# Performance work log

Hardware: AMD Instinct MI355X
Metric: run time of the kernel (lower is better)

The kernel has to match this reference:

```python
import jax, jax.numpy as jnp
import numpy as np

B, S, D_IN, D_HEAD = 4, 4096, 1024, 64

def setup_inputs() -> dict:
    key = jax.random.key(0)
    k1, k2, k3, k4 = jax.random.split(key, 4)
    scale = 0.02
    return {
        "input_vectors": jax.random.normal(k1, (B, S, D_IN), dtype=jnp.float32),
        "Wq": jax.random.normal(k2, (D_IN, D_HEAD), dtype=jnp.float32) * scale,
        "Wk": jax.random.normal(k3, (D_IN, D_HEAD), dtype=jnp.float32) * scale,
        "Wv": jax.random.normal(k4, (D_IN, D_HEAD), dtype=jnp.float32) * scale,
    }

def reference(input_vectors, Wq, Wk, Wv):
    # QKV projections (Linear with no bias): [B,S,d_in] @ [d_in,d_head]
    q = input_vectors @ Wq  # [B,S,H]
    k = input_vectors @ Wk
    v = input_vectors @ Wv
    n = input_vectors.shape[1]
    # causal attention scores: [B,S,S]
    scores = jnp.einsum('bqh,bkh->bqk', q, k)
    causal = jnp.tril(jnp.ones((n, n), dtype=bool))  # True = keep
    scores = jnp.where(causal, scores, -jnp.inf)
    scale = k.shape[-1] ** -0.5
    attn = jax.nn.softmax(scores * scale, axis=-1)
    return jnp.einsum('bqk,bkh->bqh', attn, v)
```

## Files before the change

kernel.cpp:

```cpp
#include <hip/hip_runtime.h>
#include <stdint.h>

#define SEQ   4096
#define DIN   1024

typedef __attribute__((ext_vector_type(8))) short bf16x8;
typedef __attribute__((ext_vector_type(4))) float floatx4;
typedef __attribute__((ext_vector_type(4))) unsigned short ushortx4;

#if __has_builtin(__builtin_amdgcn_exp2f)
#define EXP2(x) __builtin_amdgcn_exp2f(x)
#else
#define EXP2(x) exp2f(x)
#endif

__device__ __forceinline__ unsigned short f2bf(float f) {
    union { float f; unsigned int u; } v; v.f = f;
    unsigned int u = v.u + 0x7fffu + ((v.u >> 16) & 1u);
    return (unsigned short)(u >> 16);
}
__device__ __forceinline__ float bf2f(unsigned short h) {
    union { unsigned int u; float f; } v; v.u = ((unsigned int)h) << 16;
    return v.f;
}
__device__ __forceinline__ float uasf(unsigned int u) {
    union { unsigned int u; float f; } v; v.u = u; return v.f;
}
__device__ __forceinline__ unsigned int fasu(float f) {
    union { float f; unsigned int u; } v; v.f = f; return v.u;
}
__device__ __forceinline__ float dpp_xor1(float x) {
    return uasf((unsigned)__builtin_amdgcn_mov_dpp((int)fasu(x), 0xB1, 0xF, 0xF, true));
}
__device__ __forceinline__ float dpp_xor2(float x) {
    return uasf((unsigned)__builtin_amdgcn_mov_dpp((int)fasu(x), 0x4E, 0xF, 0xF, true));
}

__global__ void wt_prep(const float* __restrict__ Wq, const float* __restrict__ Wk,
                        const float* __restrict__ Wv, unsigned short* __restrict__ WT) {
    int idx = blockIdx.x * 256 + threadIdx.x;
    int n   = idx & 63;
    int k   = (idx >> 6) & 1023;
    int mat = idx >> 16;
    const float* W = (mat == 0) ? Wq : ((mat == 1) ? Wk : Wv);
    WT[(size_t)(mat * 64 + n) * 1024 + k] = f2bf(W[k * 64 + n]);
}

#define QSCALE 0.18033688011112042f
__launch_bounds__(512, 2)
__global__ void proj_qkv(const float* __restrict__ X, const unsigned short* __restrict__ WT,
                         unsigned short* __restrict__ qb, unsigned short* __restrict__ kb,
                         unsigned short* __restrict__ vb) {
    __shared__ __align__(16) float          X0[64 * 64], X1[64 * 64];
    __shared__ __align__(16) unsigned short W0[192 * 64], W1[192 * 64];
    const int tid = threadIdx.x;
    const int wave = tid >> 6, lane = tid & 63;
    const int quad = lane >> 4, l16 = lane & 15;
    const int strip = wave >> 1;
    const int cg = wave & 1;
    const int row0 = blockIdx.x * 64;
    const int m = strip * 16 + l16;

    floatx4 acc[6];
#pragma unroll
    for (int i = 0; i < 6; i++) acc[i] = (floatx4){0.f, 0.f, 0.f, 0.f};

    int xu[2], xr[2], xc[2], wu[3], wr[3], wc[3];
#pragma unroll
    for (int i = 0; i < 2; i++) {
        xu[i] = i * 512 + tid; xr[i] = xu[i] >> 4; xc[i] = (xu[i] & 15) ^ (xr[i] & 15);
    }
#pragma unroll
    for (int i = 0; i < 3; i++) {
        wu[i] = i * 512 + tid; wr[i] = wu[i] >> 3; wc[i] = (wu[i] & 7) ^ (wr[i] & 7);
    }
    floatx4 xpre[2], wpre[3];
    auto issue = [&](int k0) {
#pragma unroll
        for (int i = 0; i < 2; i++)
            xpre[i] = *(const floatx4*)(X + (size_t)(row0 + xr[i]) * DIN + k0 + xc[i] * 4);
#pragma unroll
        for (int i = 0; i < 3; i++)
            wpre[i] = *(const floatx4*)(WT + (size_t)wr[i] * 1024 + k0 + wc[i] * 8);
    };

    issue(0);
    for (int kc = 0; kc < 16; kc++) {
        float*          Xd = (kc & 1) ? X1 : X0;
        unsigned short* Wd = (kc & 1) ? W1 : W0;
#pragma unroll
        for (int i = 0; i < 2; i++) *(floatx4*)&Xd[xu[i] * 4] = xpre[i];
#pragma unroll
        for (int i = 0; i < 3; i++) *(floatx4*)&Wd[wu[i] * 8] = wpre[i];
        if (kc < 15) issue((kc + 1) * 64);
        __syncthreads();

        bf16x8 af[2];
#pragma unroll
        for (int ks = 0; ks < 2; ks++) {
            floatx4 x0 = *(const floatx4*)&Xd[m * 64 + ((ks * 8 + quad * 2 + 0) ^ (m & 15)) * 4];
            floatx4 x1 = *(const floatx4*)&Xd[m * 64 + ((ks * 8 + quad * 2 + 1) ^ (m & 15)) * 4];
#pragma unroll
            for (int j = 0; j < 4; j++) {
                af[ks][j]     = (short)f2bf(x0[j]);
                af[ks][j + 4] = (short)f2bf(x1[j]);
            }
        }
#pragma unroll
        for (int i = 0; i < 6; i++) {
            const int nrow = (cg * 6 + i) * 16 + l16;
#pragma unroll
            for (int ks = 0; ks < 2; ks++) {
                const int c = ks * 4 + quad;
                bf16x8 bfrag = *(const bf16x8*)&Wd[nrow * 64 + (c ^ (nrow & 7)) * 8];
                acc[i] = __builtin_amdgcn_mfma_f32_16x16x32_bf16(af[ks], bfrag, acc[i], 0, 0, 0);
            }
        }
    }
#pragma unroll
    for (int i = 0; i < 6; i++) {
        const int nt = cg * 6 + i;
        const int mat = nt >> 2;
        const int col = (nt & 3) * 16 + l16;
#pragma unroll
        for (int r = 0; r < 4; r++) {
            const int orow = row0 + strip * 16 + quad * 4 + r;
            float v = acc[i][r];
            if (mat == 0) {
                qb[(size_t)orow * 64 + col] = f2bf(v * QSCALE);
            } else if (mat == 1) {
                kb[(size_t)orow * 64 + col] = f2bf(v);
            } else {
                int b = orow >> 12, sq = orow & 4095;
                vb[((size_t)b * 64 + col) * SEQ + sq] = f2bf(v);
            }
        }
    }
}

__launch_bounds__(256, 2)
__global__ void attn(const unsigned short* __restrict__ qb, const unsigned short* __restrict__ kb,
                     const unsigned short* __restrict__ vb, unsigned short* __restrict__ opart,
                     float* __restrict__ lpart) {
    __shared__ __align__(16) unsigned short K0[64 * 64], K1[64 * 64];
    __shared__ __align__(16) unsigned short V0[64 * 64], V1[64 * 64];
    __shared__ __align__(16) unsigned short Pl[4][32 * 72];

    const int bid = blockIdx.x;
    const int batch = bid & 3;
    const int mm = bid >> 2;
    const int rank = (bid < 256) ? (127 - mm) : (mm - 64);
    const int qt = rank >> 2, s = rank & 3;
    const int q0 = qt * 128;
    const int T = 2 * qt + 2;
    const int ktlo = (T * s) >> 2, kthi = (T * (s + 1)) >> 2;

    const int tid = threadIdx.x;
    const int wave = tid >> 6, lane = tid & 63;
    const int quad = lane >> 4, l16 = lane & 15;

    bf16x8 qa[2][2];
#pragma unroll
    for (int rt = 0; rt < 2; rt++) {
        const unsigned short* qr = qb + (size_t)(batch * SEQ + q0 + wave * 32 + rt * 16 + l16) * 64;
        qa[rt][0] = *(const bf16x8*)(qr + quad * 8);
        qa[rt][1] = *(const bf16x8*)(qr + 32 + quad * 8);
    }
    floatx4 o[2][4];
#pragma unroll
    for (int rt = 0; rt < 2; rt++)
#pragma unroll
        for (int nt = 0; nt < 4; nt++) o[rt][nt] = (floatx4){0.f, 0.f, 0.f, 0.f};
    float lsum[2] = {0.f, 0.f};

    const unsigned short* kbase = kb + (size_t)batch * SEQ * 64;
    const unsigned short* vbase = vb + (size_t)batch * 64 * SEQ;

    int ku[2], kr[2], kc_[2], vu[2], vd[2], vc[2];
#pragma unroll
    for (int i = 0; i < 2; i++) {
        ku[i] = i * 256 + tid; kr[i] = ku[i] >> 3; kc_[i] = (ku[i] & 7) ^ (kr[i] & 7);
        vu[i] = i * 256 + tid; vd[i] = vu[i] >> 3; vc[i] = (vu[i] & 7) ^ (vd[i] & 7);
    }
    floatx4 kpre[2], vpre[2];
    auto issue = [&](int k0) {
#pragma unroll
        for (int i = 0; i < 2; i++)
            kpre[i] = *(const floatx4*)(kbase + (size_t)(k0 + kr[i]) * 64 + kc_[i] * 8);
#pragma unroll
        for (int i = 0; i < 2; i++)
            vpre[i] = *(const floatx4*)(vbase + (size_t)vd[i] * SEQ + k0 + vc[i] * 8);
    };

    if (ktlo < kthi) issue(ktlo * 64);
    for (int kt = ktlo; kt < kthi; kt++) {
        unsigned short* Kd = (kt & 1) ? K1 : K0;
        unsigned short* Vd = (kt & 1) ? V1 : V0;
#pragma unroll
        for (int i = 0; i < 2; i++) *(floatx4*)&Kd[ku[i] * 8] = kpre[i];
#pragma unroll
        for (int i = 0; i < 2; i++) *(floatx4*)&Vd[vu[i] * 8] = vpre[i];
        if (kt + 1 < kthi) issue((kt + 1) * 64);
        __syncthreads();

        const int k0 = kt * 64;
        const bool domask = (k0 + 63) > (q0 + wave * 32);
        unsigned short* P = &Pl[wave][0];
#pragma unroll
        for (int rt = 0; rt < 2; rt++) {
            floatx4 sc[4];
#pragma unroll
            for (int nt = 0; nt < 4; nt++) {
                sc[nt] = (floatx4){0.f, 0.f, 0.f, 0.f};
                const int key = nt * 16 + l16;
#pragma unroll
                for (int ks = 0; ks < 2; ks++) {
                    const int c = ks * 4 + quad;
                    bf16x8 bk = *(const bf16x8*)&Kd[key * 64 + (c ^ (key & 7)) * 8];
                    sc[nt] = __builtin_amdgcn_mfma_f32_16x16x32_bf16(qa[rt][ks], bk, sc[nt], 0, 0, 0);
                }
            }
            if (domask) {
#pragma unroll
                for (int nt = 0; nt < 4; nt++) {
                    const int col = k0 + nt * 16 + l16;
#pragma unroll
                    for (int r = 0; r < 4; r++) {
                        const int rowg = q0 + wave * 32 + rt * 16 + quad * 4 + r;
                        if (col > rowg) sc[nt][r] = -1e30f;
                    }
                }
            }
#pragma unroll
            for (int nt = 0; nt < 4; nt++) {
                float v0 = EXP2(sc[nt][0]), v1 = EXP2(sc[nt][1]);
                float v2 = EXP2(sc[nt][2]), v3 = EXP2(sc[nt][3]);
                float t0 = dpp_xor2(v0), t1 = dpp_xor2(v1), t2 = dpp_xor2(v2), t3 = dpp_xor2(v3);
                if (lane & 2) { v0 = t2; v1 = t3; } else { v2 = t0; v3 = t1; }
                t0 = dpp_xor1(v0); t1 = dpp_xor1(v1); t2 = dpp_xor1(v2); t3 = dpp_xor1(v3);
                if (lane & 1) { v0 = t1; v2 = t3; } else { v1 = t0; v3 = t2; }
                unsigned int u0 = fasu(v0) & 0xffff0000u, u1 = fasu(v1) & 0xffff0000u;
                unsigned int u2 = fasu(v2) & 0xffff0000u, u3 = fasu(v3) & 0xffff0000u;
                lsum[rt] += (uasf(u0) + uasf(u1)) + (uasf(u2) + uasf(u3));
                uint2 w;
                w.x = (u0 >> 16) | u1;
                w.y = (u2 >> 16) | u3;
                const int prow = rt * 16 + quad * 4 + (lane & 3);
                const int pcol = nt * 16 + (l16 >> 2) * 4;
                *(uint2*)&P[prow * 72 + pcol] = w;
            }
        }
#pragma unroll
        for (int ks = 0; ks < 2; ks++) {
            bf16x8 pa[2];
#pragma unroll
            for (int rt = 0; rt < 2; rt++)
                pa[rt] = *(const bf16x8*)&P[(rt * 16 + l16) * 72 + ks * 32 + quad * 8];
#pragma unroll
            for (int nt = 0; nt < 4; nt++) {
                const int d = nt * 16 + l16;
                bf16x8 bv = *(const bf16x8*)&Vd[d * 64 + (((ks * 4 + quad)) ^ (d & 7)) * 8];
#pragma unroll
                for (int rt = 0; rt < 2; rt++)
                    o[rt][nt] = __builtin_amdgcn_mfma_f32_16x16x32_bf16(pa[rt], bv, o[rt][nt], 0, 0, 0);
            }
        }
    }

    unsigned short* ob = opart + (size_t)s * (4 * SEQ * 64)
                       + (size_t)(batch * SEQ + q0 + wave * 32) * 64;
    float* lb = lpart + (size_t)s * (4 * SEQ) + (size_t)(batch * SEQ + q0 + wave * 32);
#pragma unroll
    for (int rt = 0; rt < 2; rt++) {
        float l = lsum[rt];
        l += __shfl_xor(l, 4);
        l += __shfl_xor(l, 8);
#pragma unroll
        for (int nt = 0; nt < 4; nt++)
#pragma unroll
            for (int r = 0; r < 4; r++)
                ob[(rt * 16 + quad * 4 + r) * 64 + nt * 16 + l16] = f2bf(o[rt][nt][r]);
        if ((l16 >> 2) == 0) lb[rt * 16 + quad * 4 + (l16 & 3)] = l;
    }
}

__global__ void merge(const unsigned short* __restrict__ opart, const float* __restrict__ lpart,
                      float* __restrict__ out) {
    int idx = blockIdx.x * 256 + threadIdx.x;
    int row = idx >> 4, c4 = idx & 15;
    float l = lpart[row] + lpart[4 * SEQ + row] + lpart[8 * SEQ + row] + lpart[12 * SEQ + row];
    float inv = 1.f / l;
    floatx4 acc = (floatx4){0.f, 0.f, 0.f, 0.f};
#pragma unroll
    for (int s = 0; s < 4; s++) {
        ushortx4 u = *(const ushortx4*)(opart + (size_t)s * (4 * SEQ * 64)
                                        + (size_t)row * 64 + c4 * 4);
#pragma unroll
        for (int j = 0; j < 4; j++) acc[j] += bf2f(u[j]);
    }
    acc *= inv;
    *(floatx4*)(out + (size_t)row * 64 + c4 * 4) = acc;
}

extern "C" void kernel_launch(void* const* d_in, const int* in_sizes, int n_in,
                              void* d_out, int out_size, void* d_ws, size_t ws_size,
                              hipStream_t stream) {
    const float* X  = (const float*)d_in[0];
    const float* Wq = (const float*)d_in[1];
    const float* Wk = (const float*)d_in[2];
    const float* Wv = (const float*)d_in[3];
    float* out = (float*)d_out;
    char* ws = (char*)d_ws;
    unsigned short* WT = (unsigned short*)ws;
    unsigned short* qb = (unsigned short*)(ws + 393216);
    unsigned short* kb = (unsigned short*)(ws + 393216 + 2097152);
    unsigned short* vb = (unsigned short*)(ws + 393216 + 2 * 2097152);
    unsigned short* opart = (unsigned short*)(ws + 393216 + 3 * 2097152);
    float* lpart = (float*)(ws + 393216 + 3 * 2097152 + 8388608);

    hipLaunchKernelGGL(wt_prep,  dim3(768), dim3(256), 0, stream, Wq, Wk, Wv, WT);
    hipLaunchKernelGGL(proj_qkv, dim3(256), dim3(512), 0, stream, X, WT, qb, kb, vb);
    hipLaunchKernelGGL(attn,     dim3(512), dim3(256), 0, stream, qb, kb, vb, opart, lpart);
    hipLaunchKernelGGL(merge,    dim3(1024), dim3(256), 0, stream, opart, lpart, out);
}
```

Before: 139.9 us.

## Fuse all stages into one persistent kernel with grid barriers and dynamic work queue

Result: slower. 261.3 us (+86.8%).

```diff
diff --git a/kernel.cpp b/kernel.cpp
--- a/kernel.cpp
+++ b/kernel.cpp
@@ -3,6 +3,8 @@
 
 #define SEQ   4096
 #define DIN   1024
+#define NBLK  256
+#define NITEMS 1024
 
 typedef __attribute__((ext_vector_type(8))) short bf16x8;
 typedef __attribute__((ext_vector_type(4))) float floatx4;
@@ -36,270 +38,268 @@
     return uasf((unsigned)__builtin_amdgcn_mov_dpp((int)fasu(x), 0x4E, 0xF, 0xF, true));
 }
 
-__global__ void wt_prep(const float* __restrict__ Wq, const float* __restrict__ Wk,
-                        const float* __restrict__ Wv, unsigned short* __restrict__ WT) {
-    int idx = blockIdx.x * 256 + threadIdx.x;
-    int n   = idx & 63;
-    int k   = (idx >> 6) & 1023;
-    int mat = idx >> 16;
-    const float* W = (mat == 0) ? Wq : ((mat == 1) ? Wk : Wv);
-    WT[(size_t)(mat * 64 + n) * 1024 + k] = f2bf(W[k * 64 + n]);
+__device__ __forceinline__ void gbar(unsigned int* c, int tid) {
+    __syncthreads();
+    if (tid == 0) {
+        __threadfence();
+        __hip_atomic_fetch_add(c, 1u, __ATOMIC_RELEASE, __HIP_MEMORY_SCOPE_AGENT);
+        while (__hip_atomic_load(c, __ATOMIC_ACQUIRE, __HIP_MEMORY_SCOPE_AGENT) < NBLK)
+            __builtin_amdgcn_s_sleep(1);
+    }
+    __syncthreads();
 }
 
 #define QSCALE 0.18033688011112042f
-__launch_bounds__(512, 2)
-__global__ void proj_qkv(const float* __restrict__ X, const unsigned short* __restrict__ WT,
-                         unsigned short* __restrict__ qb, unsigned short* __restrict__ kb,
-                         unsigned short* __restrict__ vb) {
-    __shared__ __align__(16) float          X0[64 * 64], X1[64 * 64];
-    __shared__ __align__(16) unsigned short W0[192 * 64], W1[192 * 64];
-    const int tid = threadIdx.x;
+
+__launch_bounds__(512, 4)
+__global__ void mega(const float* __restrict__ X, const float* __restrict__ Wq,
+                     const float* __restrict__ Wk, const float* __restrict__ Wv,
+                     unsigned short* __restrict__ WT, unsigned short* __restrict__ qb,
+                     unsigned short* __restrict__ kb, unsigned short* __restrict__ vb,
+                     unsigned short* __restrict__ opart, float* __restrict__ lpart,
+                     unsigned int* cnt, float* __restrict__ out) {
+    __shared__ __align__(16) char smem[81920];
+    const int tid = threadIdx.x, bid = blockIdx.x;
     const int wave = tid >> 6, lane = tid & 63;
     const int quad = lane >> 4, l16 = lane & 15;
-    const int strip = wave >> 1;
-    const int cg = wave & 1;
-    const int row0 = blockIdx.x * 64;
-    const int m = strip * 16 + l16;
-
-    floatx4 acc[6];
-#pragma unroll
-    for (int i = 0; i < 6; i++) acc[i] = (floatx4){0.f, 0.f, 0.f, 0.f};
-
-    int xu[2], xr[2], xc[2], wu[3], wr[3], wc[3];
-#pragma unroll
-    for (int i = 0; i < 2; i++) {
-        xu[i] = i * 512 + tid; xr[i] = xu[i] >> 4; xc[i] = (xu[i] & 15) ^ (xr[i] & 15);
-    }
-#pragma unroll
-    for (int i = 0; i < 3; i++) {
-        wu[i] = i * 512 + tid; wr[i] = wu[i] >> 3; wc[i] = (wu[i] & 7) ^ (wr[i] & 7);
-    }
-    floatx4 xpre[2], wpre[3];
-    auto issue = [&](int k0) {
-#pragma unroll
-        for (int i = 0; i < 2; i++)
-            xpre[i] = *(const floatx4*)(X + (size_t)(row0 + xr[i]) * DIN + k0 + xc[i] * 4);
-#pragma unroll
-        for (int i = 0; i < 3; i++)
-            wpre[i] = *(const floatx4*)(WT + (size_t)wr[i] * 1024 + k0 + wc[i] * 8);
-    };
-
-    issue(0);
-    for (int kc = 0; kc < 16; kc++) {
-        float*          Xd = (kc & 1) ? X1 : X0;
-        unsigned short* Wd = (kc & 1) ? W1 : W0;
-#pragma unroll
-        for (int i = 0; i < 2; i++) *(floatx4*)&Xd[xu[i] * 4] = xpre[i];
-#pragma unroll
-        for (int i = 0; i < 3; i++) *(floatx4*)&Wd[wu[i] * 8] = wpre[i];
-        if (kc < 15) issue((kc + 1) * 64);
-        __syncthreads();
-
-        bf16x8 af[2];
-#pragma unroll
-        for (int ks = 0; ks < 2; ks++) {
-            floatx4 x0 = *(const floatx4*)&Xd[m * 64 + ((ks * 8 + quad * 2 + 0) ^ (m & 15)) * 4];
-            floatx4 x1 = *(const floatx4*)&Xd[m * 64 + ((ks * 8 + quad * 2 + 1) ^ (m & 15)) * 4];
-#pragma unroll
-            for (int j = 0; j < 4; j++) {
-                af[ks][j]     = (short)f2bf(x0[j]);
-                af[ks][j + 4] = (short)f2bf(x1[j]);
-            }
-        }
-#pragma unroll
-        for (int i = 0; i < 6; i++) {
-            const int nrow = (cg * 6 + i) * 16 + l16;
+
+    for (int idx = bid * 512 + tid; idx < 196608; idx += 131072) {
+        int k = idx & 1023, n = (idx >> 10) & 63, mat = idx >> 16;
+        const float* W = (mat == 0) ? Wq : ((mat == 1) ? Wk : Wv);
+        WT[idx] = f2bf(W[k * 64 + n]);
+    }
+    gbar(cnt + 0, tid);
+
+    {
+        float*          X0 = (float*)smem;
+        float*          X1 = (float*)(smem + 16384);
+        unsigned short* W0 = (unsigned short*)(smem + 32768);
+        unsigned short* W1 = (unsigned short*)(smem + 57344);
+        const int strip = wave >> 1, cg = wave & 1;
+        const int row0 = bid * 64;
+        const int m = strip * 16 + l16;
+
+        floatx4 acc[6];
+#pragma unroll
+        for (int i = 0; i < 6; i++) acc[i] = (floatx4){0.f, 0.f, 0.f, 0.f};
+
+        int xu[2], xr[2], xc[2], wu[3], wr[3], wc[3];
+#pragma unroll
+        for (int i = 0; i < 2; i++) {
+            xu[i] = i * 512 + tid; xr[i] = xu[i] >> 4; xc[i] = (xu[i] & 15) ^ (xr[i] & 15);
+        }
+#pragma unroll
+        for (int i = 0; i < 3; i++) {
+            wu[i] = i * 512 + tid; wr[i] = wu[i] >> 3; wc[i] = (wu[i] & 7) ^ (wr[i] & 7);
+        }
+        floatx4 xpre[2], wpre[3];
+        auto issue = [&](int k0) {
+#pragma unroll
+            for (int i = 0; i < 2; i++)
+                xpre[i] = *(const floatx4*)(X + (size_t)(row0 + xr[i]) * DIN + k0 + xc[i] * 4);
+#pragma unroll
+            for (int i = 0; i < 3; i++)
+                wpre[i] = *(const floatx4*)(WT + (size_t)wr[i] * 1024 + k0 + wc[i] * 8);
+        };
+
+        issue(0);
+        for (int kc = 0; kc < 16; kc++) {
+            float*          Xd = (kc & 1) ? X1 : X0;
+            unsigned short* Wd = (kc & 1) ? W1 : W0;
+#pragma unroll
+            for (int i = 0; i < 2; i++) *(floatx4*)&Xd[xu[i] * 4] = xpre[i];
+#pragma unroll
+            for (int i = 0; i < 3; i++) *(floatx4*)&Wd[wu[i] * 8] = wpre[i];
+            if (kc < 15) issue((kc + 1) * 64);
+            __syncthreads();
+
+            bf16x8 af[2];
 #pragma unroll
             for (int ks = 0; ks < 2; ks++) {
-                const int c = ks * 4 + quad;
-                bf16x8 bfrag = *(const bf16x8*)&Wd[nrow * 64 + (c ^ (nrow & 7)) * 8];
-                acc[i] = __builtin_amdgcn_mfma_f32_16x16x32_bf16(af[ks], bfrag, acc[i], 0, 0, 0);
-            }
-        }
-    }
-#pragma unroll
-    for (int i = 0; i < 6; i++) {
-        const int nt = cg * 6 + i;
-        const int mat = nt >> 2;
-        const int col = (nt & 3) * 16 + l16;
-#pragma unroll
-        for (int r = 0; r < 4; r++) {
-            const int orow = row0 + strip * 16 + quad * 4 + r;
-            float v = acc[i][r];
-            if (mat == 0) {
-                qb[(size_t)orow * 64 + col] = f2bf(v * QSCALE);
-            } else if (mat == 1) {
-                kb[(size_t)orow * 64 + col] = f2bf(v);
-            } else {
-                int b = orow >> 12, sq = orow & 4095;
-                vb[((size_t)b * 64 + col) * SEQ + sq] = f2bf(v);
-            }
-        }
-    }
-}
-
-__launch_bounds__(256, 2)
-__global__ void attn(const unsigned short* __restrict__ qb, const unsigned short* __restrict__ kb,
-                     const unsigned short* __restrict__ vb, unsigned short* __restrict__ opart,
-                     float* __restrict__ lpart) {
-    __shared__ __align__(16) unsigned short K0[64 * 64], K1[64 * 64];
-    __shared__ __align__(16) unsigned short V0[64 * 64], V1[64 * 64];
-    __shared__ __align__(16) unsigned short Pl[4][32 * 72];
-
-    const int bid = blockIdx.x;
-    const int batch = bid & 3;
-    const int mm = bid >> 2;
-    const int rank = (bid < 256) ? (127 - mm) : (mm - 64);
-    const int qt = rank >> 2, s = rank & 3;
-    const int q0 = qt * 128;
-    const int T = 2 * qt + 2;
-    const int ktlo = (T * s) >> 2, kthi = (T * (s + 1)) >> 2;
-
-    const int tid = threadIdx.x;
-    const int wave = tid >> 6, lane = tid & 63;
-    const int quad = lane >> 4, l16 = lane & 15;
-
-    bf16x8 qa[2][2];
-#pragma unroll
-    for (int rt = 0; rt < 2; rt++) {
-        const unsigned short* qr = qb + (size_t)(batch * SEQ + q0 + wave * 32 + rt * 16 + l16) * 64;
-        qa[rt][0] = *(const bf16x8*)(qr + quad * 8);
-        qa[rt][1] = *(const bf16x8*)(qr + 32 + quad * 8);
-    }
-    floatx4 o[2][4];
-#pragma unroll
-    for (int rt = 0; rt < 2; rt++)
-#pragma unroll
-        for (int nt = 0; nt < 4; nt++) o[rt][nt] = (floatx4){0.f, 0.f, 0.f, 0.f};
-    float lsum[2] = {0.f, 0.f};
-
-    const unsigned short* kbase = kb + (size_t)batch * SEQ * 64;
-    const unsigned short* vbase = vb + (size_t)batch * 64 * SEQ;
-
-    int ku[2], kr[2], kc_[2], vu[2], vd[2], vc[2];
-#pragma unroll
-    for (int i = 0; i < 2; i++) {
-        ku[i] = i * 256 + tid; kr[i] = ku[i] >> 3; kc_[i] = (ku[i] & 7) ^ (kr[i] & 7);
-        vu[i] = i * 256 + tid; vd[i] = vu[i] >> 3; vc[i] = (vu[i] & 7) ^ (vd[i] & 7);
-    }
-    floatx4 kpre[2], vpre[2];
-    auto issue = [&](int k0) {
-#pragma unroll
-        for (int i = 0; i < 2; i++)
-            kpre[i] = *(const floatx4*)(kbase + (size_t)(k0 + kr[i]) * 64 + kc_[i] * 8);
-#pragma unroll
-        for (int i = 0; i < 2; i++)
-            vpre[i] = *(const floatx4*)(vbase + (size_t)vd[i] * SEQ + k0 + vc[i] * 8);
-    };
-
-    if (ktlo < kthi) issue(ktlo * 64);
-    for (int kt = ktlo; kt < kthi; kt++) {
-        unsigned short* Kd = (kt & 1) ? K1 : K0;
-        unsigned short* Vd = (kt & 1) ? V1 : V0;
-#pragma unroll
-        for (int i = 0; i < 2; i++) *(floatx4*)&Kd[ku[i] * 8] = kpre[i];
-#pragma unroll
-        for (int i = 0; i < 2; i++) *(floatx4*)&Vd[vu[i] * 8] = vpre[i];
-        if (kt + 1 < kthi) issue((kt + 1) * 64);
-        __syncthreads();
-
-        const int k0 = kt * 64;
-        const bool domask = (k0 + 63) > (q0 + wave * 32);
-        unsigned short* P = &Pl[wave][0];
-#pragma unroll
-        for (int rt = 0; rt < 2; rt++) {
-            floatx4 sc[4];
-#pragma unroll
-            for (int nt = 0; nt < 4; nt++) {
-                sc[nt] = (floatx4){0.f, 0.f, 0.f, 0.f};
-                const int key = nt * 16 + l16;
+                floatx4 x0 = *(const floatx4*)&Xd[m * 64 + ((ks * 8 + quad * 2 + 0) ^ (m & 15)) * 4];
+                floatx4 x1 = *(const floatx4*)&Xd[m * 64 + ((ks * 8 + quad * 2 + 1) ^ (m & 15)) * 4];
+#pragma unroll
+                for (int j = 0; j < 4; j++) {
+                    af[ks][j]     = (short)f2bf(x0[j]);
+                    af[ks][j + 4] = (short)f2bf(x1[j]);
+                }
+            }
+#pragma unroll
+            for (int i = 0; i < 6; i++) {
+                const int nrow = (cg * 6 + i) * 16 + l16;
 #pragma unroll
                 for (int ks = 0; ks < 2; ks++) {
                     const int c = ks * 4 + quad;
-                    bf16x8 bk = *(const bf16x8*)&Kd[key * 64 + (c ^ (key & 7)) * 8];
-                    sc[nt] = __builtin_amdgcn_mfma_f32_16x16x32_bf16(qa[rt][ks], bk, sc[nt], 0, 0, 0);
-                }
-            }
-            if (domask) {
+                    bf16x8 bfrag = *(const bf16x8*)&Wd[nrow * 64 + (c ^ (nrow & 7)) * 8];
+                    acc[i] = __builtin_amdgcn_mfma_f32_16x16x32_bf16(af[ks], bfrag, acc[i], 0, 0, 0);
+                }
+            }
+        }
+#pragma unroll
+        for (int i = 0; i < 6; i++) {
+            const int nt = cg * 6 + i;
+            const int mat = nt >> 2;
+            const int col = (nt & 3) * 16 + l16;
+#pragma unroll
+            for (int r = 0; r < 4; r++) {
+                const int orow = row0 + strip * 16 + quad * 4 + r;
+                float v = acc[i][r];
+                if (mat == 0) {
+                    qb[(size_t)orow * 64 + col] = f2bf(v * QSCALE);
+                } else if (mat == 1) {
+                    kb[(size_t)orow * 64 + col] = f2bf(v);
+                } else {
+                    int b = orow >> 12, sq = orow & 4095;
+                    vb[((size_t)b * 64 + col) * SEQ + sq] = f2bf(v);
+                }
+            }
+        }
+    }
+    gbar(cnt + 1, tid);
+
+    {
+        unsigned short* K0 = (unsigned short*)smem;
+        unsigned short* K1 = (unsigned short*)(smem + 8192);
+        unsigned short* V0 = (unsigned short*)(smem + 16384);
+        unsigned short* V1 = (unsigned short*)(smem + 24576);
+        unsigned short* Pb = (unsigned short*)(smem + 32768);
+        int* item_s = (int*)(smem + 51200);
+        unsigned short* P = Pb + wave * (16 * 72);
+
+        const int ku = tid, kr = ku >> 3, kc_ = (ku & 7) ^ (kr & 7);
+        const int vu = tid, vd = vu >> 3, vc = (vu & 7) ^ (vd & 7);
+
+        for (;;) {
+            __syncthreads();
+            if (tid == 0) *item_s = (int)atomicAdd(cnt + 3, 1u);
+            __syncthreads();
+            const int it = *item_s;
+            if (it >= NITEMS) break;
+            const int qt = 31 - (it >> 5);
+            const int batch = (it >> 3) & 3;
+            const int s = it & 7;
+            const int T = 2 * qt + 2;
+            const int lo = (T * s) >> 3, hi = (T * (s + 1)) >> 3;
+            if (lo == hi) continue;
+
+            const int q0 = qt * 128;
+            const unsigned short* kbase = kb + (size_t)batch * SEQ * 64;
+            const unsigned short* vbase = vb + (size_t)batch * 64 * SEQ;
+            const unsigned short* qr = qb + (size_t)(batch * SEQ + q0 + wave * 16 + l16) * 64;
+            bf16x8 qa0 = *(const bf16x8*)(qr + quad * 8);
+            bf16x8 qa1 = *(const bf16x8*)(qr + 32 + quad * 8);
+
+            floatx4 o[4];
+#pragma unroll
+            for (int i = 0; i < 4; i++) o[i] = (floatx4){0.f, 0.f, 0.f, 0.f};
+            float lsum = 0.f;
+
+            floatx4 kpre, vpre;
+            auto issue = [&](int k0) {
+                kpre = *(const floatx4*)(kbase + (size_t)(k0 + kr) * 64 + kc_ * 8);
+                vpre = *(const floatx4*)(vbase + (size_t)vd * SEQ + k0 + vc * 8);
+            };
+
+            issue(lo * 64);
+            for (int kt = lo; kt < hi; kt++) {
+                unsigned short* Kd = (kt & 1) ? K1 : K0;
+                unsigned short* Vd = (kt & 1) ? V1 : V0;
+                *(floatx4*)&Kd[ku * 8] = kpre;
+                *(floatx4*)&Vd[vu * 8] = vpre;
+                if (kt + 1 < hi) issue((kt + 1) * 64);
+                __syncthreads();
+
+                const int k0 = kt * 64;
+                floatx4 sc[4];
 #pragma unroll
                 for (int nt = 0; nt < 4; nt++) {
-                    const int col = k0 + nt * 16 + l16;
-#pragma unroll
-                    for (int r = 0; r < 4; r++) {
-                        const int rowg = q0 + wave * 32 + rt * 16 + quad * 4 + r;
-                        if (col > rowg) sc[nt][r] = -1e30f;
+                    sc[nt] = (floatx4){0.f, 0.f, 0.f, 0.f};
+                    const int key = nt * 16 + l16;
+#pragma unroll
+                    for (int ks = 0; ks < 2; ks++) {
+                        const int c = ks * 4 + quad;
+                        bf16x8 bk = *(const bf16x8*)&Kd[key * 64 + (c ^ (key & 7)) * 8];
+                        sc[nt] = __builtin_amdgcn_mfma_f32_16x16x32_bf16(
+                            ks == 0 ? qa0 : qa1, bk, sc[nt], 0, 0, 0);
                     }
                 }
-            }
-#pragma unroll
-            for (int nt = 0; nt < 4; nt++) {
-                float v0 = EXP2(sc[nt][0]), v1 = EXP2(sc[nt][1]);
-                float v2 = EXP2(sc[nt][2]), v3 = EXP2(sc[nt][3]);
-                float t0 = dpp_xor2(v0), t1 = dpp_xor2(v1), t2 = dpp_xor2(v2), t3 = dpp_xor2(v3);
-                if (lane & 2) { v0 = t2; v1 = t3; } else { v2 = t0; v3 = t1; }
-                t0 = dpp_xor1(v0); t1 = dpp_xor1(v1); t2 = dpp_xor1(v2); t3 = dpp_xor1(v3);
-                if (lane & 1) { v0 = t1; v2 = t3; } else { v1 = t0; v3 = t2; }
-                unsigned int u0 = fasu(v0) & 0xffff0000u, u1 = fasu(v1) & 0xffff0000u;
-                unsigned int u2 = fasu(v2) & 0xffff0000u, u3 = fasu(v3) & 0xffff0000u;
-                lsum[rt] += (uasf(u0) + uasf(u1)) + (uasf(u2) + uasf(u3));
-                uint2 w;
-                w.x = (u0 >> 16) | u1;
-                w.y = (u2 >> 16) | u3;
-                const int prow = rt * 16 + quad * 4 + (lane & 3);
-                const int pcol = nt * 16 + (l16 >> 2) * 4;
-                *(uint2*)&P[prow * 72 + pcol] = w;
-            }
-        }
-#pragma unroll
-        for (int ks = 0; ks < 2; ks++) {
-            bf16x8 pa[2];
-#pragma unroll
-            for (int rt = 0; rt < 2; rt++)
-                pa[rt] = *(const bf16x8*)&P[(rt * 16 + l16) * 72 + ks * 32 + quad * 8];
-#pragma unroll
-            for (int nt = 0; nt < 4; nt++) {
-                const int d = nt * 16 + l16;
-                bf16x8 bv = *(const bf16x8*)&Vd[d * 64 + (((ks * 4 + quad)) ^ (d & 7)) * 8];
-#pragma unroll
-                for (int rt = 0; rt < 2; rt++)
-                    o[rt][nt] = __builtin_amdgcn_mfma_f32_16x16x32_bf16(pa[rt], bv, o[rt][nt], 0, 0, 0);
-            }
-        }
-    }
-
-    unsigned short* ob = opart + (size_t)s * (4 * SEQ * 64)
-                       + (size_t)(batch * SEQ + q0 + wave * 32) * 64;
-    float* lb = lpart + (size_t)s * (4 * SEQ) + (size_t)(batch * SEQ + q0 + wave * 32);
-#pragma unroll
-    for (int rt = 0; rt < 2; rt++) {
-        float l = lsum[rt];
-        l += __shfl_xor(l, 4);
-        l += __shfl_xor(l, 8);
-#pragma unroll
-        for (int nt = 0; nt < 4; nt++)
-#pragma unroll
-            for (int r = 0; r < 4; r++)
-                ob[(rt * 16 + quad * 4 + r) * 64 + nt * 16 + l16] = f2bf(o[rt][nt][r]);
-        if ((l16 >> 2) == 0) lb[rt * 16 + quad * 4 + (l16 & 3)] = l;
-    }
-}
-
-__global__ void merge(const unsigned short* __restrict__ opart, const float* __restrict__ lpart,
-                      float* __restrict__ out) {
-    int idx = blockIdx.x * 256 + threadIdx.x;
-    int row = idx >> 4, c4 = idx & 15;
-    float l = lpart[row] + lpart[4 * SEQ + row] + lpart[8 * SEQ + row] + lpart[12 * SEQ + row];
-    float inv = 1.f / l;
-    floatx4 acc = (floatx4){0.f, 0.f, 0.f, 0.f};
-#pragma unroll
-    for (int s = 0; s < 4; s++) {
-        ushortx4 u = *(const ushortx4*)(opart + (size_t)s * (4 * SEQ * 64)
-                                        + (size_t)row * 64 + c4 * 4);
-#pragma unroll
-        for (int j = 0; j < 4; j++) acc[j] += bf2f(u[j]);
-    }
-    acc *= inv;
-    *(floatx4*)(out + (size_t)row * 64 + c4 * 4) = acc;
+                if (k0 + 63 > q0 + wave * 16) {
+#pragma unroll
+                    for (int nt = 0; nt < 4; nt++) {
+                        const int col = k0 + nt * 16 + l16;
+#pragma unroll
+                        for (int r = 0; r < 4; r++) {
+                            const int rowg = q0 + wave * 16 + quad * 4 + r;
+                            if (col > rowg) sc[nt][r] = -1e30f;
+                        }
+                    }
+                }
+#pragma unroll
+                for (int nt = 0; nt < 4; nt++) {
+                    float v0 = EXP2(sc[nt][0]), v1 = EXP2(sc[nt][1]);
+                    float v2 = EXP2(sc[nt][2]), v3 = EXP2(sc[nt][3]);
+                    float t0 = dpp_xor2(v0), t1 = dpp_xor2(v1), t2 = dpp_xor2(v2), t3 = dpp_xor2(v3);
+                    if (lane & 2) { v0 = t2; v1 = t3; } else { v2 = t0; v3 = t1; }
+                    t0 = dpp_xor1(v0); t1 = dpp_xor1(v1); t2 = dpp_xor1(v2); t3 = dpp_xor1(v3);
+                    if (lane & 1) { v0 = t1; v2 = t3; } else { v1 = t0; v3 = t2; }
+                    unsigned int u0 = fasu(v0) & 0xffff0000u, u1 = fasu(v1) & 0xffff0000u;
+                    unsigned int u2 = fasu(v2) & 0xffff0000u, u3 = fasu(v3) & 0xffff0000u;
+                    lsum += (uasf(u0) + uasf(u1)) + (uasf(u2) + uasf(u3));
+                    uint2 w;
+                    w.x = (u0 >> 16) | u1;
+                    w.y = (u2 >> 16) | u3;
+                    const int prow = quad * 4 + (lane & 3);
+                    const int pcol = nt * 16 + (l16 >> 2) * 4;
+                    *(uint2*)&P[prow * 72 + pcol] = w;
+                }
+#pragma unroll
+                for (int ks = 0; ks < 2; ks++) {
+                    bf16x8 pa = *(const bf16x8*)&P[l16 * 72 + ks * 32 + quad * 8];
+#pragma unroll
+                    for (int nt = 0; nt < 4; nt++) {
+                        const int d = nt * 16 + l16;
+                        bf16x8 bv = *(const bf16x8*)&Vd[d * 64 + ((ks * 4 + quad) ^ (d & 7)) * 8];
+                        o[nt] = __builtin_amdgcn_mfma_f32_16x16x32_bf16(pa, bv, o[nt], 0, 0, 0);
+                    }
+                }
+            }
+
+            unsigned short* ob = opart + (size_t)s * (4 * SEQ * 64)
+                               + (size_t)(batch * SEQ + q0 + wave * 16) * 64;
+            float* lb = lpart + (size_t)s * (4 * SEQ) + (batch * SEQ + q0 + wave * 16);
+            float l = lsum;
+            l += __shfl_xor(l, 4);
+            l += __shfl_xor(l, 8);
+#pragma unroll
+            for (int nt = 0; nt < 4; nt++)
+#pragma unroll
+                for (int r = 0; r < 4; r++)
+                    ob[(quad * 4 + r) * 64 + nt * 16 + l16] = f2bf(o[nt][r]);
+            if ((l16 >> 2) == 0) lb[quad * 4 + (lane & 3)] = l;
+        }
+    }
+    gbar(cnt + 2, tid);
+
+    for (int u = bid * 512 + tid; u < 262144; u += 131072) {
+        const int row = u >> 4, c4 = u & 15;
+        const int qt = (row & 4095) >> 7;
+        const int T = 2 * qt + 2;
+        float l = 0.f;
+        floatx4 acc = (floatx4){0.f, 0.f, 0.f, 0.f};
+#pragma unroll
+        for (int s = 0; s < 8; s++) {
+            const int lo = (T * s) >> 3, hi = (T * (s + 1)) >> 3;
+            if (lo < hi) {
+                l += lpart[s * (4 * SEQ) + row];
+                ushortx4 v = *(const ushortx4*)(opart + (size_t)s * (4 * SEQ * 64)
+                                                + (size_t)row * 64 + c4 * 4);
+#pragma unroll
+                for (int j = 0; j < 4; j++) acc[j] += bf2f(v[j]);
+            }
+        }
+        acc *= (1.f / l);
+        *(floatx4*)(out + (size_t)row * 64 + c4 * 4) = acc;
+    }
 }
 
 extern "C" void kernel_launch(void* const* d_in, const int* in_sizes, int n_in,
@@ -311,15 +311,15 @@
     const float* Wv = (const float*)d_in[3];
     float* out = (float*)d_out;
     char* ws = (char*)d_ws;
-    unsigned short* WT = (unsigned short*)ws;
-    unsigned short* qb = (unsigned short*)(ws + 393216);
-    unsigned short* kb = (unsigned short*)(ws + 393216 + 2097152);
-    unsigned short* vb = (unsigned short*)(ws + 393216 + 2 * 2097152);
-    unsigned short* opart = (unsigned short*)(ws + 393216 + 3 * 2097152);
-    float* lpart = (float*)(ws + 393216 + 3 * 2097152 + 8388608);
-
-    hipLaunchKernelGGL(wt_prep,  dim3(768), dim3(256), 0, stream, Wq, Wk, Wv, WT);
-    hipLaunchKernelGGL(proj_qkv, dim3(256), dim3(512), 0, stream, X, WT, qb, kb, vb);
-    hipLaunchKernelGGL(attn,     dim3(512), dim3(256), 0, stream, qb, kb, vb, opart, lpart);
-    hipLaunchKernelGGL(merge,    dim3(1024), dim3(256), 0, stream, opart, lpart, out);
-}
+    unsigned short* WT    = (unsigned short*)(ws + 0);
+    unsigned short* qb    = (unsigned short*)(ws + 393216);
+    unsigned short* kb    = (unsigned short*)(ws + 2490368);
+    unsigned short* vb    = (unsigned short*)(ws + 4587520);
+    unsigned short* opart = (unsigned short*)(ws + 6684672);
+    float*          lpart = (float*)(ws + 23461888);
+    unsigned int*   cnt   = (unsigned int*)(ws + 23986176);
+
+    hipMemsetAsync(cnt, 0, 16, stream);
+    hipLaunchKernelGGL(mega, dim3(NBLK), dim3(512), 0, stream,
+                       X, Wq, Wk, Wv, WT, qb, kb, vb, opart, lpart, cnt, out);
+}
```

## Shrink attention query tile to 64 rows, single-buffer K/V, raise occupancy

Applied to the files above, without the earlier changes.

After: 135.0 us. 3.5% less time.

```diff
diff --git a/kernel.cpp b/kernel.cpp
--- a/kernel.cpp
+++ b/kernel.cpp
@@ -39,11 +39,11 @@
 __global__ void wt_prep(const float* __restrict__ Wq, const float* __restrict__ Wk,
                         const float* __restrict__ Wv, unsigned short* __restrict__ WT) {
     int idx = blockIdx.x * 256 + threadIdx.x;
-    int n   = idx & 63;
-    int k   = (idx >> 6) & 1023;
+    int k   = idx & 1023;
+    int n   = (idx >> 10) & 63;
     int mat = idx >> 16;
     const float* W = (mat == 0) ? Wq : ((mat == 1) ? Wk : Wv);
-    WT[(size_t)(mat * 64 + n) * 1024 + k] = f2bf(W[k * 64 + n]);
+    WT[idx] = f2bf(W[k * 64 + n]);
 }
 
 #define QSCALE 0.18033688011112042f
@@ -138,43 +138,38 @@
     }
 }
 
-__launch_bounds__(256, 2)
+__launch_bounds__(256, 4)
 __global__ void attn(const unsigned short* __restrict__ qb, const unsigned short* __restrict__ kb,
                      const unsigned short* __restrict__ vb, unsigned short* __restrict__ opart,
                      float* __restrict__ lpart) {
-    __shared__ __align__(16) unsigned short K0[64 * 64], K1[64 * 64];
-    __shared__ __align__(16) unsigned short V0[64 * 64], V1[64 * 64];
-    __shared__ __align__(16) unsigned short Pl[4][32 * 72];
+    __shared__ __align__(16) unsigned short Kl[64 * 64];
+    __shared__ __align__(16) unsigned short Vl[64 * 64];
+    __shared__ __align__(16) unsigned short Pl[4][16 * 72];
 
     const int bid = blockIdx.x;
-    const int batch = bid & 3;
-    const int mm = bid >> 2;
-    const int rank = (bid < 256) ? (127 - mm) : (mm - 64);
-    const int qt = rank >> 2, s = rank & 3;
-    const int q0 = qt * 128;
-    const int T = 2 * qt + 2;
-    const int ktlo = (T * s) >> 2, kthi = (T * (s + 1)) >> 2;
+    const int qt = 63 - (bid >> 4);
+    const int batch = (bid >> 2) & 3;
+    const int s = bid & 3;
+    const int q0 = qt * 64;
+    const int T = qt + 1;
+    const int lo = (T * s) >> 2, hi = (T * (s + 1)) >> 2;
 
     const int tid = threadIdx.x;
     const int wave = tid >> 6, lane = tid & 63;
     const int quad = lane >> 4, l16 = lane & 15;
 
-    bf16x8 qa[2][2];
-#pragma unroll
-    for (int rt = 0; rt < 2; rt++) {
-        const unsigned short* qr = qb + (size_t)(batch * SEQ + q0 + wave * 32 + rt * 16 + l16) * 64;
-        qa[rt][0] = *(const bf16x8*)(qr + quad * 8);
-        qa[rt][1] = *(const bf16x8*)(qr + 32 + quad * 8);
-    }
-    floatx4 o[2][4];
-#pragma unroll
-    for (int rt = 0; rt < 2; rt++)
-#pragma unroll
-        for (int nt = 0; nt < 4; nt++) o[rt][nt] = (floatx4){0.f, 0.f, 0.f, 0.f};
-    float lsum[2] = {0.f, 0.f};
+    const unsigned short* qr = qb + (size_t)(batch * SEQ + q0 + wave * 16 + l16) * 64;
+    bf16x8 qa0 = *(const bf16x8*)(qr + quad * 8);
+    bf16x8 qa1 = *(const bf16x8*)(qr + 32 + quad * 8);
+
+    floatx4 o[4];
+#pragma unroll
+    for (int i = 0; i < 4; i++) o[i] = (floatx4){0.f, 0.f, 0.f, 0.f};
+    float lsum = 0.f;
 
     const unsigned short* kbase = kb + (size_t)batch * SEQ * 64;
     const unsigned short* vbase = vb + (size_t)batch * 64 * SEQ;
+    unsigned short* P = &Pl[wave][0];
 
     int ku[2], kr[2], kc_[2], vu[2], vd[2], vc[2];
 #pragma unroll
@@ -192,96 +187,83 @@
             vpre[i] = *(const floatx4*)(vbase + (size_t)vd[i] * SEQ + k0 + vc[i] * 8);
     };
 
-    if (ktlo < kthi) issue(ktlo * 64);
-    for (int kt = ktlo; kt < kthi; kt++) {
-        unsigned short* Kd = (kt & 1) ? K1 : K0;
-        unsigned short* Vd = (kt & 1) ? V1 : V0;
-#pragma unroll
-        for (int i = 0; i < 2; i++) *(floatx4*)&Kd[ku[i] * 8] = kpre[i];
-#pragma unroll
-        for (int i = 0; i < 2; i++) *(floatx4*)&Vd[vu[i] * 8] = vpre[i];
-        if (kt + 1 < kthi) issue((kt + 1) * 64);
+    if (lo < hi) issue(lo * 64);
+    for (int kt = lo; kt < hi; kt++) {
         __syncthreads();
+#pragma unroll
+        for (int i = 0; i < 2; i++) *(floatx4*)&Kl[ku[i] * 8] = kpre[i];
+#pragma unroll
+        for (int i = 0; i < 2; i++) *(floatx4*)&Vl[vu[i] * 8] = vpre[i];
+        if (kt + 1 < hi) issue((kt + 1) * 64);
+        __syncthreads();
 
         const int k0 = kt * 64;
-        const bool domask = (k0 + 63) > (q0 + wave * 32);
-        unsigned short* P = &Pl[wave][0];
-#pragma unroll
-        for (int rt = 0; rt < 2; rt++) {
-            floatx4 sc[4];
+        floatx4 sc[4];
+#pragma unroll
+        for (int nt = 0; nt < 4; nt++) {
+            sc[nt] = (floatx4){0.f, 0.f, 0.f, 0.f};
+            const int key = nt * 16 + l16;
+#pragma unroll
+            for (int ks = 0; ks < 2; ks++) {
+                const int c = ks * 4 + quad;
+                bf16x8 bk = *(const bf16x8*)&Kl[key * 64 + (c ^ (key & 7)) * 8];
+                sc[nt] = __builtin_amdgcn_mfma_f32_16x16x32_bf16(
+                    ks == 0 ? qa0 : qa1, bk, sc[nt], 0, 0, 0);
+            }
+        }
+        if (kt == T - 1) {
 #pragma unroll
             for (int nt = 0; nt < 4; nt++) {
-                sc[nt] = (floatx4){0.f, 0.f, 0.f, 0.f};
-                const int key = nt * 16 + l16;
-#pragma unroll
-                for (int ks = 0; ks < 2; ks++) {
-                    const int c = ks * 4 + quad;
-                    bf16x8 bk = *(const bf16x8*)&Kd[key * 64 + (c ^ (key & 7)) * 8];
-                    sc[nt] = __builtin_amdgcn_mfma_f32_16x16x32_bf16(qa[rt][ks], bk, sc[nt], 0, 0, 0);
+                const int col = k0 + nt * 16 + l16;
+#pragma unroll
+                for (int r = 0; r < 4; r++) {
+                    const int rowg = q0 + wave * 16 + quad * 4 + r;
+                    if (col > rowg) sc[nt][r] = -1e30f;
                 }
             }
-            if (domask) {
-#pragma unroll
-                for (int nt = 0; nt < 4; nt++) {
-                    const int col = k0 + nt * 16 + l16;
-#pragma unroll
-                    for (int r = 0; r < 4; r++) {
-                        const int rowg = q0 + wave * 32 + rt * 16 + quad * 4 + r;
-                        if (col > rowg) sc[nt][r] = -1e30f;
-                    }
-                }
-            }
-#pragma unroll
-            for (int nt = 0; nt < 4; nt++) {
-                float v0 = EXP2(sc[nt][0]), v1 = EXP2(sc[nt][1]);
-                float v2 = EXP2(sc[nt][2]), v3 = EXP2(sc[nt][3]);
-                float t0 = dpp_xor2(v0), t1 = dpp_xor2(v1), t2 = dpp_xor2(v2), t3 = dpp_xor2(v3);
-                if (lane & 2) { v0 = t2; v1 = t3; } else { v2 = t0; v3 = t1; }
-                t0 = dpp_xor1(v0); t1 = dpp_xor1(v1); t2 = dpp_xor1(v2); t3 = dpp_xor1(v3);
-                if (lane & 1) { v0 = t1; v2 = t3; } else { v1 = t0; v3 = t2; }
-                unsigned int u0 = fasu(v0) & 0xffff0000u, u1 = fasu(v1) & 0xffff0000u;
-                unsigned int u2 = fasu(v2) & 0xffff0000u, u3 = fasu(v3) & 0xffff0000u;
-                lsum[rt] += (uasf(u0) + uasf(u1)) + (uasf(u2) + uasf(u3));
-                uint2 w;
-                w.x = (u0 >> 16) | u1;
-                w.y = (u2 >> 16) | u3;
-                const int prow = rt * 16 + quad * 4 + (lane & 3);
-                const int pcol = nt * 16 + (l16 >> 2) * 4;
-                *(uint2*)&P[prow * 72 + pcol] = w;
-            }
+        }
+#pragma unroll
+        for (int nt = 0; nt < 4; nt++) {
+            float v0 = EXP2(sc[nt][0]), v1 = EXP2(sc[nt][1]);
+            float v2 = EXP2(sc[nt][2]), v3 = EXP2(sc[nt][3]);
+            float t0 = dpp_xor2(v0), t1 = dpp_xor2(v1), t2 = dpp_xor2(v2), t3 = dpp_xor2(v3);
+            if (lane & 2) { v0 = t2; v1 = t3; } else { v2 = t0; v3 = t1; }
+            t0 = dpp_xor1(v0); t1 = dpp_xor1(v1); t2 = dpp_xor1(v2); t3 = dpp_xor1(v3);
+            if (lane & 1) { v0 = t1; v2 = t3; } else { v1 = t0; v3 = t2; }
+            unsigned int u0 = fasu(v0) & 0xffff0000u, u1 = fasu(v1) & 0xffff0000u;
+            unsigned int u2 = fasu(v2) & 0xffff0000u, u3 = fasu(v3) & 0xffff0000u;
+            lsum += (uasf(u0) + uasf(u1)) + (uasf(u2) + uasf(u3));
+            uint2 w;
+            w.x = (u0 >> 16) | u1;
+            w.y = (u2 >> 16) | u3;
+            const int prow = quad * 4 + (lane & 3);
+            const int pcol = nt * 16 + (l16 >> 2) * 4;
+            *(uint2*)&P[prow * 72 + pcol] = w;
         }
 #pragma unroll
         for (int ks = 0; ks < 2; ks++) {
-            bf16x8 pa[2];
-#pragma unroll
-            for (int rt = 0; rt < 2; rt++)
-                pa[rt] = *(const bf16x8*)&P[(rt * 16 + l16) * 72 + ks * 32 + quad * 8];
+            bf16x8 pa = *(const bf16x8*)&P[l16 * 72 + ks * 32 + quad * 8];
 #pragma unroll
             for (int nt = 0; nt < 4; nt++) {
                 const int d = nt * 16 + l16;
-                bf16x8 bv = *(const bf16x8*)&Vd[d * 64 + (((ks * 4 + quad)) ^ (d & 7)) * 8];
-#pragma unroll
-                for (int rt = 0; rt < 2; rt++)
-                    o[rt][nt] = __builtin_amdgcn_mfma_f32_16x16x32_bf16(pa[rt], bv, o[rt][nt], 0, 0, 0);
+                bf16x8 bv = *(const bf16x8*)&Vl[d * 64 + ((ks * 4 + quad) ^ (d & 7)) * 8];
+                o[nt] = __builtin_amdgcn_mfma_f32_16x16x32_bf16(pa, bv, o[nt], 0, 0, 0);
             }
         }
     }
 
     unsigned short* ob = opart + (size_t)s * (4 * SEQ * 64)
-                       + (size_t)(batch * SEQ + q0 + wave * 32) * 64;
-    float* lb = lpart + (size_t)s * (4 * SEQ) + (size_t)(batch * SEQ + q0 + wave * 32);
-#pragma unroll
-    for (int rt = 0; rt < 2; rt++) {
-        float l = lsum[rt];
-        l += __shfl_xor(l, 4);
-        l += __shfl_xor(l, 8);
-#pragma unroll
-        for (int nt = 0; nt < 4; nt++)
-#pragma unroll
-            for (int r = 0; r < 4; r++)
-                ob[(rt * 16 + quad * 4 + r) * 64 + nt * 16 + l16] = f2bf(o[rt][nt][r]);
-        if ((l16 >> 2) == 0) lb[rt * 16 + quad * 4 + (l16 & 3)] = l;
-    }
+                       + (size_t)(batch * SEQ + q0 + wave * 16) * 64;
+    float* lb = lpart + (size_t)s * (4 * SEQ) + (batch * SEQ + q0 + wave * 16);
+    float l = lsum;
+    l += __shfl_xor(l, 4);
+    l += __shfl_xor(l, 8);
+#pragma unroll
+    for (int nt = 0; nt < 4; nt++)
+#pragma unroll
+        for (int r = 0; r < 4; r++)
+            ob[(quad * 4 + r) * 64 + nt * 16 + l16] = f2bf(o[nt][r]);
+    if ((l16 >> 2) == 0) lb[quad * 4 + (lane & 3)] = l;
 }
 
 __global__ void merge(const unsigned short* __restrict__ opart, const float* __restrict__ lpart,
@@ -311,15 +293,15 @@
     const float* Wv = (const float*)d_in[3];
     float* out = (float*)d_out;
     char* ws = (char*)d_ws;
-    unsigned short* WT = (unsigned short*)ws;
-    unsigned short* qb = (unsigned short*)(ws + 393216);
-    unsigned short* kb = (unsigned short*)(ws + 393216 + 2097152);
-    unsigned short* vb = (unsigned short*)(ws + 393216 + 2 * 2097152);
-    unsigned short* opart = (unsigned short*)(ws + 393216 + 3 * 2097152);
-    float* lpart = (float*)(ws + 393216 + 3 * 2097152 + 8388608);
-
-    hipLaunchKernelGGL(wt_prep,  dim3(768), dim3(256), 0, stream, Wq, Wk, Wv, WT);
-    hipLaunchKernelGGL(proj_qkv, dim3(256), dim3(512), 0, stream, X, WT, qb, kb, vb);
-    hipLaunchKernelGGL(attn,     dim3(512), dim3(256), 0, stream, qb, kb, vb, opart, lpart);
+    unsigned short* WT    = (unsigned short*)(ws + 0);
+    unsigned short* qb    = (unsigned short*)(ws + 393216);
+    unsigned short* kb    = (unsigned short*)(ws + 2490368);
+    unsigned short* vb    = (unsigned short*)(ws + 4587520);
+    unsigned short* opart = (unsigned short*)(ws + 6684672);
+    float*          lpart = (float*)(ws + 15073280);
+
+    hipLaunchKernelGGL(wt_prep,  dim3(768),  dim3(256), 0, stream, Wq, Wk, Wv, WT);
+    hipLaunchKernelGGL(proj_qkv, dim3(256),  dim3(512), 0, stream, X, WT, qb, kb, vb);
+    hipLaunchKernelGGL(attn,     dim3(1024), dim3(256), 0, stream, qb, kb, vb, opart, lpart);
     hipLaunchKernelGGL(merge,    dim3(1024), dim3(256), 0, stream, opart, lpart, out);
 }
```
